# Kernel tuning notes

Measured on AMD Instinct MI355X. Metric: run time of the kernel, lower is better.

The kernel has to match this reference:

```python
import jax, jax.numpy as jnp
import numpy as np

SAMPLE_RATE = 16000
HUM_FREQ = 60
Q_FACTOR = 30.0
BATCH = 128
SAMPLES = 160000


def _notch_sos(freq, Q, fs):
    # scipy.signal.iirnotch closed form (gb = 1/sqrt(2) -> beta = tan(bw/2))
    w0 = 2.0 * np.pi * freq / fs
    beta = np.tan(w0 / (2.0 * Q))
    gain = 1.0 / (1.0 + beta)
    b0 = gain
    b1 = -2.0 * gain * np.cos(w0)
    b2 = gain
    a1 = -2.0 * gain * np.cos(w0)
    a2 = 2.0 * gain - 1.0
    # tf2sos of a 2nd-order TF: single section [b0,b1,b2,a0=1,a1,a2]
    return [b0, b1, b2, 1.0, a1, a2]


def _build_sos():
    rows = []
    for f in (HUM_FREQ, HUM_FREQ * 2, HUM_FREQ * 3):
        if f < SAMPLE_RATE / 2:
            rows.append(_notch_sos(f, Q_FACTOR, SAMPLE_RATE))
    return np.asarray(rows, dtype=np.float32)  # [3, 6]


def setup_inputs() -> dict:
    key = jax.random.key(0)
    audio = jax.random.normal(key, (BATCH, SAMPLES), dtype=jnp.float32)
    sos = jnp.asarray(_build_sos())  # [n_sections, 6], a0 == 1
    return {"audio": audio, "sos": sos}


def _sosfilt(sos, x):
    """Cascaded biquad IIR (direct form II transposed), matching scipy.sosfilt.
    sos: [n_sections, 6] with a0 == 1.  x: [B, T].  Returns [B, T].
    """
    n_sections = sos.shape[0]
    B = x.shape[0]

    def step(z, xt):  # z: [n_sections, 2, B], xt: [B]
        y = xt
        new_z = []
        for s in range(n_sections):
            b0, b1, b2 = sos[s, 0], sos[s, 1], sos[s, 2]
            a1, a2 = sos[s, 4], sos[s, 5]
            out = b0 * y + z[s, 0]
            z0 = b1 * y - a1 * out + z[s, 1]
            z1 = b2 * y - a2 * out
            new_z.append(jnp.stack([z0, z1]))
            y = out
        return jnp.stack(new_z), y

    z_init = jnp.zeros((n_sections, 2, B), dtype=x.dtype)
    _, ys = jax.lax.scan(step, z_init, x.T)  # ys: [T, B]
    return ys.T


def reference(audio, sos):
    squeeze = audio.ndim == 1
    a = audio[None, :] if squeeze else audio
    y = _sosfilt(sos, a)
    return y[0] if squeeze else y
```

## Files before the change

### kernel.cpp

```cpp
#include <hip/hip_runtime.h>

typedef float vfloat4 __attribute__((ext_vector_type(4)));

#define B_ROWS 128
#define T_SAMP 160000
#define NSEC 3
#define LCH 20
#define NF4 5
#define RST 21
#define SUPW 1280
#define NSUP 125
#define NSC (B_ROWS * NSUP)
#define WPB 4

struct Coefs { float b0[NSEC], b1[NSEC], b2[NSEC], a1[NSEC], a2[NSEC]; };

__device__ __forceinline__ void load_coefs(const float* __restrict__ sos, Coefs& c) {
#pragma unroll
  for (int s = 0; s < NSEC; ++s) {
    c.b0[s] = sos[s * 6 + 0];
    c.b1[s] = sos[s * 6 + 1];
    c.b2[s] = sos[s * 6 + 2];
    c.a1[s] = sos[s * 6 + 4];
    c.a2[s] = sos[s * 6 + 5];
  }
}

__device__ __forceinline__ float df2t_step(const Coefs& c, float z[6], float x) {
  float y = x;
#pragma unroll
  for (int s = 0; s < NSEC; ++s) {
    float out = fmaf(c.b0[s], y, z[2 * s]);
    float t0  = fmaf(c.b1[s], y, z[2 * s + 1]);
    z[2 * s]     = fmaf(-c.a1[s], out, t0);
    float t1  = c.b2[s] * y;
    z[2 * s + 1] = fmaf(-c.a2[s], out, t1);
    y = out;
  }
  return y;
}

__device__ __forceinline__ void tri_combine(float f[6], const float* __restrict__ P,
                                            const float t[6]) {
  float nf[6];
#pragma unroll
  for (int e = 0; e < 6; ++e) {
    float acc = f[e];
    const int kmax = ((e >> 1) << 1) + 2;
#pragma unroll
    for (int kk = 0; kk < 6; ++kk)
      if (kk < kmax) acc = fmaf(P[e * 6 + kk], t[kk], acc);
    nf[e] = acc;
  }
#pragma unroll
  for (int e = 0; e < 6; ++e) f[e] = nf[e];
}

__device__ __forceinline__ float dmm6(float a, float b, int i, int j) {
  float s = 0.f;
#pragma unroll
  for (int k = 0; k < 6; ++k)
    s = fmaf(__shfl(a, i * 6 + k), __shfl(b, k * 6 + j), s);
  return s;
}

__global__ __launch_bounds__(64) void setup_kernel(const float* __restrict__ sos,
                                                   float* __restrict__ mats) {
  __shared__ float Ash[36];
  __shared__ float As5[5 * 36];
  const int lane = threadIdx.x;
  Coefs cf; load_coefs(sos, cf);
  if (lane == 0) {
    float A[36];
#pragma unroll
    for (int jc = 0; jc < 6; ++jc) {
      float z[6] = {0.f, 0.f, 0.f, 0.f, 0.f, 0.f};
      z[jc] = 1.f;
      df2t_step(cf, z, 0.f);
#pragma unroll
      for (int ic = 0; ic < 6; ++ic) A[ic * 6 + jc] = z[ic];
    }
#pragma unroll
    for (int q = 0; q < 36; ++q) Ash[q] = A[q];
  }
  __syncthreads();

  const int e = (lane < 36) ? lane : 0;
  const int mi = e / 6, mj = e % 6;
  float a1p = Ash[e];
  float a2p  = dmm6(a1p, a1p, mi, mj);
  float a4p  = dmm6(a2p, a2p, mi, mj);
  float a8p  = dmm6(a4p, a4p, mi, mj);
  float a16p = dmm6(a8p, a8p, mi, mj);
  if (lane < 36) {
    As5[lane] = a1p; As5[36 + lane] = a2p; As5[72 + lane] = a4p;
    As5[108 + lane] = a8p; As5[144 + lane] = a16p;
  }
  float pk = dmm6(a16p, a4p, mi, mj);
  if (lane < 36) mats[lane] = pk;
#pragma unroll
  for (int k = 1; k < 6; ++k) {
    pk = dmm6(pk, pk, mi, mj);
    if (lane < 36) mats[k * 36 + lane] = pk;
  }
  float q = dmm6(pk, pk, mi, mj);
  if (lane < 36) mats[216 + lane] = q;
#pragma unroll
  for (int k = 1; k < 7; ++k) {
    q = dmm6(q, q, mi, mj);
    if (lane < 36) mats[216 + k * 36 + lane] = q;
  }
  if (lane < LCH) {
    float g[6] = {cf.b0[1] * cf.b0[2], 0.f, cf.b0[2], 0.f, 1.f, 0.f};
#pragma unroll
    for (int k = 0; k < 5; ++k) {
      if (lane & (1 << k)) {
        float ng[6];
#pragma unroll
        for (int j = 0; j < 6; ++j) {
          float acc = 0.f;
#pragma unroll
          for (int i = 0; i < 6; ++i) acc = fmaf(g[i], As5[k * 36 + i * 6 + j], acc);
          ng[j] = acc;
        }
#pragma unroll
        for (int j = 0; j < 6; ++j) g[j] = ng[j];
      }
    }
#pragma unroll
    for (int j = 0; j < 6; ++j) mats[468 + lane * 6 + j] = g[j];
  }
}

__global__ __launch_bounds__(256) void pass1_kernel(const float* __restrict__ x,
                                                    const float* __restrict__ sos,
                                                    const float* __restrict__ mats,
                                                    float* __restrict__ Fsup) {
  const int tid = threadIdx.x, w = tid >> 6, lane = tid & 63;
  Coefs cf; load_coefs(sos, cf);
  const int S = blockIdx.x * WPB + w;
  const int r = S / NSUP, s = S - r * NSUP;
  const float4* src = reinterpret_cast<const float4*>(
      x + (size_t)r * T_SAMP + (size_t)s * SUPW + (size_t)lane * LCH);
  float4 v0 = src[0], v1 = src[1], v2 = src[2], v3 = src[3], v4 = src[4];

  float f[6] = {0.f, 0.f, 0.f, 0.f, 0.f, 0.f};
  df2t_step(cf, f, v0.x); df2t_step(cf, f, v0.y); df2t_step(cf, f, v0.z); df2t_step(cf, f, v0.w);
  df2t_step(cf, f, v1.x); df2t_step(cf, f, v1.y); df2t_step(cf, f, v1.z); df2t_step(cf, f, v1.w);
  df2t_step(cf, f, v2.x); df2t_step(cf, f, v2.y); df2t_step(cf, f, v2.z); df2t_step(cf, f, v2.w);
  df2t_step(cf, f, v3.x); df2t_step(cf, f, v3.y); df2t_step(cf, f, v3.z); df2t_step(cf, f, v3.w);
  df2t_step(cf, f, v4.x); df2t_step(cf, f, v4.y); df2t_step(cf, f, v4.z); df2t_step(cf, f, v4.w);

#pragma unroll
  for (int k = 0; k < 6; ++k) {
    float t6[6];
#pragma unroll
    for (int e = 0; e < 6; ++e) t6[e] = __shfl_up(f[e], 1 << k);
    if (lane >= (1 << k)) tri_combine(f, mats + k * 36, t6);
  }
  if (lane == 63) {
    float* fo = Fsup + (size_t)S * 6;
#pragma unroll
    for (int e = 0; e < 6; ++e) fo[e] = f[e];
  }
}

__global__ __launch_bounds__(64) void middle_scan(const float* __restrict__ Fsup,
                                                  const float* __restrict__ mats,
                                                  float* __restrict__ zsup) {
  const float* Qm = mats + 216;
  const int r = blockIdx.x, lane = threadIdx.x;
  const float* frow = Fsup + (size_t)r * NSUP * 6;
  float fc[2][6];
#pragma unroll
  for (int jj = 0; jj < 2; ++jj) {
    int c = 2 * lane + jj;
#pragma unroll
    for (int e = 0; e < 6; ++e) fc[jj][e] = (c < NSUP) ? frow[c * 6 + e] : 0.f;
  }
  float s[6] = {0.f, 0.f, 0.f, 0.f, 0.f, 0.f};
#pragma unroll
  for (int jj = 0; jj < 2; ++jj) {
    float ns[6];
#pragma unroll
    for (int e = 0; e < 6; ++e) {
      float acc = fc[jj][e];
#pragma unroll
      for (int kk = 0; kk < 6; ++kk) acc = fmaf(Qm[e * 6 + kk], s[kk], acc);
      ns[e] = acc;
    }
#pragma unroll
    for (int e = 0; e < 6; ++e) s[e] = ns[e];
  }
#pragma unroll
  for (int k = 0; k < 6; ++k) {
    float t[6];
#pragma unroll
    for (int e = 0; e < 6; ++e) t[e] = __shfl_up(s[e], 1 << k);
    if (lane >= (1 << k)) tri_combine(s, Qm + (k + 1) * 36, t);
  }
  float z[6];
#pragma unroll
  for (int e = 0; e < 6; ++e) {
    float t = __shfl_up(s[e], 1);
    z[e] = (lane == 0) ? 0.f : t;
  }
  float* zrow = zsup + (size_t)r * NSUP * 6;
#pragma unroll
  for (int jj = 0; jj < 2; ++jj) {
    int c = 2 * lane + jj;
    if (c < NSUP) {
#pragma unroll
      for (int e = 0; e < 6; ++e) zrow[c * 6 + e] = z[e];
    }
    float nz[6];
#pragma unroll
    for (int e = 0; e < 6; ++e) {
      float acc = fc[jj][e];
#pragma unroll
      for (int kk = 0; kk < 6; ++kk) acc = fmaf(Qm[e * 6 + kk], z[kk], acc);
      nz[e] = acc;
    }
#pragma unroll
    for (int e = 0; e < 6; ++e) z[e] = nz[e];
  }
}

__global__ __launch_bounds__(256) void pass2_kernel(const float* __restrict__ x,
                                                    const float* __restrict__ sos,
                                                    const float* __restrict__ mats,
                                                    const float* __restrict__ zsup,
                                                    float* __restrict__ y) {
  __shared__ float Tr[WPB][64 * RST];
  const int tid = threadIdx.x, w = tid >> 6, lane = tid & 63;
  Coefs cf; load_coefs(sos, cf);
  const int S = blockIdx.x * WPB + w;
  const int r = S / NSUP, s = S - r * NSUP;
  const size_t base = (size_t)r * T_SAMP + (size_t)s * SUPW;
  const float4* src = reinterpret_cast<const float4*>(x + base + (size_t)lane * LCH);
  float4 v0 = src[0], v1 = src[1], v2 = src[2], v3 = src[3], v4 = src[4];

  float z0[6];
  const float* zp = zsup + (size_t)S * 6;
#pragma unroll
  for (int e = 0; e < 6; ++e) z0[e] = zp[e];

  float f[6] = {0.f, 0.f, 0.f, 0.f, 0.f, 0.f};
  v0.x = df2t_step(cf, f, v0.x); v0.y = df2t_step(cf, f, v0.y);
  v0.z = df2t_step(cf, f, v0.z); v0.w = df2t_step(cf, f, v0.w);
  v1.x = df2t_step(cf, f, v1.x); v1.y = df2t_step(cf, f, v1.y);
  v1.z = df2t_step(cf, f, v1.z); v1.w = df2t_step(cf, f, v1.w);
  v2.x = df2t_step(cf, f, v2.x); v2.y = df2t_step(cf, f, v2.y);
  v2.z = df2t_step(cf, f, v2.z); v2.w = df2t_step(cf, f, v2.w);
  v3.x = df2t_step(cf, f, v3.x); v3.y = df2t_step(cf, f, v3.y);
  v3.z = df2t_step(cf, f, v3.z); v3.w = df2t_step(cf, f, v3.w);
  v4.x = df2t_step(cf, f, v4.x); v4.y = df2t_step(cf, f, v4.y);
  v4.z = df2t_step(cf, f, v4.z); v4.w = df2t_step(cf, f, v4.w);

  if (lane == 0) tri_combine(f, mats, z0);
#pragma unroll
  for (int k = 0; k < 6; ++k) {
    float t6[6];
#pragma unroll
    for (int e = 0; e < 6; ++e) t6[e] = __shfl_up(f[e], 1 << k);
    if (lane >= (1 << k)) tri_combine(f, mats + k * 36, t6);
  }
  float zs[6];
#pragma unroll
  for (int e = 0; e < 6; ++e) {
    float tt = __shfl_up(f[e], 1);
    zs[e] = (lane == 0) ? z0[e] : tt;
  }

  const float* Gm = mats + 468;
  float* myrow = &Tr[w][lane * RST];
  auto corr = [&](int tl, float yz) {
    float a = yz;
#pragma unroll
    for (int e = 0; e < 6; ++e) a = fmaf(Gm[tl * 6 + e], zs[e], a);
    myrow[tl] = a;
  };
  corr(0, v0.x);  corr(1, v0.y);  corr(2, v0.z);  corr(3, v0.w);
  corr(4, v1.x);  corr(5, v1.y);  corr(6, v1.z);  corr(7, v1.w);
  corr(8, v2.x);  corr(9, v2.y);  corr(10, v2.z); corr(11, v2.w);
  corr(12, v3.x); corr(13, v3.y); corr(14, v3.z); corr(15, v3.w);
  corr(16, v4.x); corr(17, v4.y); corr(18, v4.z); corr(19, v4.w);
  __syncthreads();

  float* dst = y + base;
#pragma unroll
  for (int i2 = 0; i2 < NF4; ++i2) {
    int q = i2 * 64 + lane, k = q / NF4, m = q - k * NF4;
    vfloat4 w4;
    w4.x = Tr[w][k * RST + m * 4 + 0];
    w4.y = Tr[w][k * RST + m * 4 + 1];
    w4.z = Tr[w][k * RST + m * 4 + 2];
    w4.w = Tr[w][k * RST + m * 4 + 3];
    __builtin_nontemporal_store(w4, reinterpret_cast<vfloat4*>(dst + 4 * q));
  }
}

extern "C" void kernel_launch(void* const* d_in, const int* in_sizes, int n_in,
                              void* d_out, int out_size, void* d_ws, size_t ws_size,
                              hipStream_t stream) {
  const float* x = (const float*)d_in[0];
  const float* sos = (const float*)d_in[1];
  float* y = (float*)d_out;

  float* Fsup = (float*)d_ws;
  float* zsup = Fsup + (size_t)NSC * 6;
  float* mats = zsup + (size_t)NSC * 6;

  hipLaunchKernelGGL(setup_kernel, dim3(1), dim3(64), 0, stream, sos, mats);
  hipLaunchKernelGGL(pass1_kernel, dim3(NSC / WPB), dim3(256), 0, stream, x, sos, mats, Fsup);
  hipLaunchKernelGGL(middle_scan, dim3(B_ROWS), dim3(64), 0, stream, Fsup, mats, zsup);
  hipLaunchKernelGGL(pass2_kernel, dim3(NSC / WPB), dim3(256), 0, stream, x, sos, mats, zsup, y);
}
```

Baseline: 63.70 us.

## Fuse setup and middle scan into the pass kernels with per-block recompute

Removes the separate setup kernel and the per-row middle scan, leaving two launches. Each block now rebuilds the state-transition matrix powers in shared memory on wave 0, overlapping that with the other waves' chunk filtering. In pass2, each wave finds its incoming state by reducing every earlier superchunk summary in its row with windowed shuffle reductions. This removes two serialized launches and a global round-trip, but repeats the matrix setup in every block and makes pass2 read up to a full row of summaries per wave. The __syncthreads before the transpose store is also dropped, which relies on each wave reading only its own shared-memory slice.

Measured after the change: 103.4 us. 1.62x slower.

```diff
diff --git a/kernel.cpp b/kernel.cpp
--- a/kernel.cpp
+++ b/kernel.cpp
@@ -64,12 +64,21 @@
   return s;
 }
 
-__global__ __launch_bounds__(64) void setup_kernel(const float* __restrict__ sos,
-                                                   float* __restrict__ mats) {
-  __shared__ float Ash[36];
-  __shared__ float As5[5 * 36];
-  const int lane = threadIdx.x;
-  Coefs cf; load_coefs(sos, cf);
+__device__ __forceinline__ void window_reduce(float val[6], const float* __restrict__ Qm,
+                                              int lane) {
+#pragma unroll
+  for (int k = 0; k < 6; ++k) {
+    float t[6];
+#pragma unroll
+    for (int e = 0; e < 6; ++e) t[e] = __shfl_down(val[e], 1 << k);
+    const bool ok = (lane + (1 << k)) < 64;
+#pragma unroll
+    for (int e = 0; e < 6; ++e) t[e] = ok ? t[e] : 0.f;
+    tri_combine(val, Qm + k * 36, t);
+  }
+}
+
+__device__ __forceinline__ float buildA_dist(const Coefs& cf, float* Ash, int lane) {
   if (lane == 0) {
     float A[36];
 #pragma unroll
@@ -83,59 +92,14 @@
 #pragma unroll
     for (int q = 0; q < 36; ++q) Ash[q] = A[q];
   }
-  __syncthreads();
-
-  const int e = (lane < 36) ? lane : 0;
-  const int mi = e / 6, mj = e % 6;
-  float a1p = Ash[e];
-  float a2p  = dmm6(a1p, a1p, mi, mj);
-  float a4p  = dmm6(a2p, a2p, mi, mj);
-  float a8p  = dmm6(a4p, a4p, mi, mj);
-  float a16p = dmm6(a8p, a8p, mi, mj);
-  if (lane < 36) {
-    As5[lane] = a1p; As5[36 + lane] = a2p; As5[72 + lane] = a4p;
-    As5[108 + lane] = a8p; As5[144 + lane] = a16p;
-  }
-  float pk = dmm6(a16p, a4p, mi, mj);
-  if (lane < 36) mats[lane] = pk;
-#pragma unroll
-  for (int k = 1; k < 6; ++k) {
-    pk = dmm6(pk, pk, mi, mj);
-    if (lane < 36) mats[k * 36 + lane] = pk;
-  }
-  float q = dmm6(pk, pk, mi, mj);
-  if (lane < 36) mats[216 + lane] = q;
-#pragma unroll
-  for (int k = 1; k < 7; ++k) {
-    q = dmm6(q, q, mi, mj);
-    if (lane < 36) mats[216 + k * 36 + lane] = q;
-  }
-  if (lane < LCH) {
-    float g[6] = {cf.b0[1] * cf.b0[2], 0.f, cf.b0[2], 0.f, 1.f, 0.f};
-#pragma unroll
-    for (int k = 0; k < 5; ++k) {
-      if (lane & (1 << k)) {
-        float ng[6];
-#pragma unroll
-        for (int j = 0; j < 6; ++j) {
-          float acc = 0.f;
-#pragma unroll
-          for (int i = 0; i < 6; ++i) acc = fmaf(g[i], As5[k * 36 + i * 6 + j], acc);
-          ng[j] = acc;
-        }
-#pragma unroll
-        for (int j = 0; j < 6; ++j) g[j] = ng[j];
-      }
-    }
-#pragma unroll
-    for (int j = 0; j < 6; ++j) mats[468 + lane * 6 + j] = g[j];
-  }
+  return Ash[(lane < 36) ? lane : 0];
 }
 
 __global__ __launch_bounds__(256) void pass1_kernel(const float* __restrict__ x,
                                                     const float* __restrict__ sos,
-                                                    const float* __restrict__ mats,
                                                     float* __restrict__ Fsup) {
+  __shared__ float Ash[36];
+  __shared__ float Pm[6 * 36];
   const int tid = threadIdx.x, w = tid >> 6, lane = tid & 63;
   Coefs cf; load_coefs(sos, cf);
   const int S = blockIdx.x * WPB + w;
@@ -144,19 +108,37 @@
       x + (size_t)r * T_SAMP + (size_t)s * SUPW + (size_t)lane * LCH);
   float4 v0 = src[0], v1 = src[1], v2 = src[2], v3 = src[3], v4 = src[4];
 
+  if (w == 0) {
+    const int e = (lane < 36) ? lane : 0;
+    const int mi = e / 6, mj = e % 6;
+    float a1p = buildA_dist(cf, Ash, lane);
+    float a2p  = dmm6(a1p, a1p, mi, mj);
+    float a4p  = dmm6(a2p, a2p, mi, mj);
+    float a8p  = dmm6(a4p, a4p, mi, mj);
+    float a16p = dmm6(a8p, a8p, mi, mj);
+    float pk = dmm6(a16p, a4p, mi, mj);
+    if (lane < 36) Pm[lane] = pk;
+#pragma unroll
+    for (int k = 1; k < 6; ++k) {
+      pk = dmm6(pk, pk, mi, mj);
+      if (lane < 36) Pm[k * 36 + lane] = pk;
+    }
+  }
+
   float f[6] = {0.f, 0.f, 0.f, 0.f, 0.f, 0.f};
   df2t_step(cf, f, v0.x); df2t_step(cf, f, v0.y); df2t_step(cf, f, v0.z); df2t_step(cf, f, v0.w);
   df2t_step(cf, f, v1.x); df2t_step(cf, f, v1.y); df2t_step(cf, f, v1.z); df2t_step(cf, f, v1.w);
   df2t_step(cf, f, v2.x); df2t_step(cf, f, v2.y); df2t_step(cf, f, v2.z); df2t_step(cf, f, v2.w);
   df2t_step(cf, f, v3.x); df2t_step(cf, f, v3.y); df2t_step(cf, f, v3.z); df2t_step(cf, f, v3.w);
   df2t_step(cf, f, v4.x); df2t_step(cf, f, v4.y); df2t_step(cf, f, v4.z); df2t_step(cf, f, v4.w);
+  __syncthreads();
 
 #pragma unroll
   for (int k = 0; k < 6; ++k) {
     float t6[6];
 #pragma unroll
     for (int e = 0; e < 6; ++e) t6[e] = __shfl_up(f[e], 1 << k);
-    if (lane >= (1 << k)) tri_combine(f, mats + k * 36, t6);
+    if (lane >= (1 << k)) tri_combine(f, Pm + k * 36, t6);
   }
   if (lane == 63) {
     float* fo = Fsup + (size_t)S * 6;
@@ -165,72 +147,15 @@
   }
 }
 
-__global__ __launch_bounds__(64) void middle_scan(const float* __restrict__ Fsup,
-                                                  const float* __restrict__ mats,
-                                                  float* __restrict__ zsup) {
-  const float* Qm = mats + 216;
-  const int r = blockIdx.x, lane = threadIdx.x;
-  const float* frow = Fsup + (size_t)r * NSUP * 6;
-  float fc[2][6];
-#pragma unroll
-  for (int jj = 0; jj < 2; ++jj) {
-    int c = 2 * lane + jj;
-#pragma unroll
-    for (int e = 0; e < 6; ++e) fc[jj][e] = (c < NSUP) ? frow[c * 6 + e] : 0.f;
-  }
-  float s[6] = {0.f, 0.f, 0.f, 0.f, 0.f, 0.f};
-#pragma unroll
-  for (int jj = 0; jj < 2; ++jj) {
-    float ns[6];
-#pragma unroll
-    for (int e = 0; e < 6; ++e) {
-      float acc = fc[jj][e];
-#pragma unroll
-      for (int kk = 0; kk < 6; ++kk) acc = fmaf(Qm[e * 6 + kk], s[kk], acc);
-      ns[e] = acc;
-    }
-#pragma unroll
-    for (int e = 0; e < 6; ++e) s[e] = ns[e];
-  }
-#pragma unroll
-  for (int k = 0; k < 6; ++k) {
-    float t[6];
-#pragma unroll
-    for (int e = 0; e < 6; ++e) t[e] = __shfl_up(s[e], 1 << k);
-    if (lane >= (1 << k)) tri_combine(s, Qm + (k + 1) * 36, t);
-  }
-  float z[6];
-#pragma unroll
-  for (int e = 0; e < 6; ++e) {
-    float t = __shfl_up(s[e], 1);
-    z[e] = (lane == 0) ? 0.f : t;
-  }
-  float* zrow = zsup + (size_t)r * NSUP * 6;
-#pragma unroll
-  for (int jj = 0; jj < 2; ++jj) {
-    int c = 2 * lane + jj;
-    if (c < NSUP) {
-#pragma unroll
-      for (int e = 0; e < 6; ++e) zrow[c * 6 + e] = z[e];
-    }
-    float nz[6];
-#pragma unroll
-    for (int e = 0; e < 6; ++e) {
-      float acc = fc[jj][e];
-#pragma unroll
-      for (int kk = 0; kk < 6; ++kk) acc = fmaf(Qm[e * 6 + kk], z[kk], acc);
-      nz[e] = acc;
-    }
-#pragma unroll
-    for (int e = 0; e < 6; ++e) z[e] = nz[e];
-  }
-}
-
 __global__ __launch_bounds__(256) void pass2_kernel(const float* __restrict__ x,
                                                     const float* __restrict__ sos,
-                                                    const float* __restrict__ mats,
-                                                    const float* __restrict__ zsup,
+                                                    const float* __restrict__ Fsup,
                                                     float* __restrict__ y) {
+  __shared__ float Ash[36];
+  __shared__ float As5[5 * 36];
+  __shared__ float Pm[6 * 36];
+  __shared__ float Qm[7 * 36];
+  __shared__ float Gm[LCH * 6];
   __shared__ float Tr[WPB][64 * RST];
   const int tid = threadIdx.x, w = tid >> 6, lane = tid & 63;
   Coefs cf; load_coefs(sos, cf);
@@ -240,10 +165,53 @@
   const float4* src = reinterpret_cast<const float4*>(x + base + (size_t)lane * LCH);
   float4 v0 = src[0], v1 = src[1], v2 = src[2], v3 = src[3], v4 = src[4];
 
-  float z0[6];
-  const float* zp = zsup + (size_t)S * 6;
-#pragma unroll
-  for (int e = 0; e < 6; ++e) z0[e] = zp[e];
+  if (w == 0) {
+    const int e = (lane < 36) ? lane : 0;
+    const int mi = e / 6, mj = e % 6;
+    float a1p = buildA_dist(cf, Ash, lane);
+    float a2p  = dmm6(a1p, a1p, mi, mj);
+    float a4p  = dmm6(a2p, a2p, mi, mj);
+    float a8p  = dmm6(a4p, a4p, mi, mj);
+    float a16p = dmm6(a8p, a8p, mi, mj);
+    if (lane < 36) {
+      As5[lane] = a1p; As5[36 + lane] = a2p; As5[72 + lane] = a4p;
+      As5[108 + lane] = a8p; As5[144 + lane] = a16p;
+    }
+    float pk = dmm6(a16p, a4p, mi, mj);
+    if (lane < 36) Pm[lane] = pk;
+#pragma unroll
+    for (int k = 1; k < 6; ++k) {
+      pk = dmm6(pk, pk, mi, mj);
+      if (lane < 36) Pm[k * 36 + lane] = pk;
+    }
+    float q = dmm6(pk, pk, mi, mj);
+    if (lane < 36) Qm[lane] = q;
+#pragma unroll
+    for (int k = 1; k < 7; ++k) {
+      q = dmm6(q, q, mi, mj);
+      if (lane < 36) Qm[k * 36 + lane] = q;
+    }
+    if (lane < LCH) {
+      float g[6] = {cf.b0[1] * cf.b0[2], 0.f, cf.b0[2], 0.f, 1.f, 0.f};
+#pragma unroll
+      for (int k = 0; k < 5; ++k) {
+        if (lane & (1 << k)) {
+          float ng[6];
+#pragma unroll
+          for (int j = 0; j < 6; ++j) {
+            float acc = 0.f;
+#pragma unroll
+            for (int i = 0; i < 6; ++i) acc = fmaf(g[i], As5[k * 36 + i * 6 + j], acc);
+            ng[j] = acc;
+          }
+#pragma unroll
+          for (int j = 0; j < 6; ++j) g[j] = ng[j];
+        }
+      }
+#pragma unroll
+      for (int j = 0; j < 6; ++j) Gm[lane * 6 + j] = g[j];
+    }
+  }
 
   float f[6] = {0.f, 0.f, 0.f, 0.f, 0.f, 0.f};
   v0.x = df2t_step(cf, f, v0.x); v0.y = df2t_step(cf, f, v0.y);
@@ -256,14 +224,44 @@
   v3.z = df2t_step(cf, f, v3.z); v3.w = df2t_step(cf, f, v3.w);
   v4.x = df2t_step(cf, f, v4.x); v4.y = df2t_step(cf, f, v4.y);
   v4.z = df2t_step(cf, f, v4.z); v4.w = df2t_step(cf, f, v4.w);
-
-  if (lane == 0) tri_combine(f, mats, z0);
+  __syncthreads();
+
+  float z0[6] = {0.f, 0.f, 0.f, 0.f, 0.f, 0.f};
+  if (s > 0) {
+    const float* frow = Fsup + (size_t)r * NSUP * 6;
+    float acc[6];
+    {
+      const int nv = (s < 64) ? s : 64;
+      const bool act = lane < nv;
+      const int c = s - 1 - lane;
+      float val[6];
+#pragma unroll
+      for (int e = 0; e < 6; ++e) val[e] = act ? frow[c * 6 + e] : 0.f;
+      window_reduce(val, Qm, lane);
+#pragma unroll
+      for (int e = 0; e < 6; ++e) acc[e] = val[e];
+    }
+    if (s > 64) {
+      const int nv = s - 64;
+      const bool act = lane < nv;
+      const int c = s - 65 - lane;
+      float val[6];
+#pragma unroll
+      for (int e = 0; e < 6; ++e) val[e] = act ? frow[c * 6 + e] : 0.f;
+      window_reduce(val, Qm, lane);
+      tri_combine(acc, Qm + 6 * 36, val);
+    }
+#pragma unroll
+    for (int e = 0; e < 6; ++e) z0[e] = __shfl(acc[e], 0);
+  }
+
+  if (lane == 0) tri_combine(f, Pm, z0);
 #pragma unroll
   for (int k = 0; k < 6; ++k) {
     float t6[6];
 #pragma unroll
     for (int e = 0; e < 6; ++e) t6[e] = __shfl_up(f[e], 1 << k);
-    if (lane >= (1 << k)) tri_combine(f, mats + k * 36, t6);
+    if (lane >= (1 << k)) tri_combine(f, Pm + k * 36, t6);
   }
   float zs[6];
 #pragma unroll
@@ -272,7 +270,6 @@
     zs[e] = (lane == 0) ? z0[e] : tt;
   }
 
-  const float* Gm = mats + 468;
   float* myrow = &Tr[w][lane * RST];
   auto corr = [&](int tl, float yz) {
     float a = yz;
@@ -285,7 +282,6 @@
   corr(8, v2.x);  corr(9, v2.y);  corr(10, v2.z); corr(11, v2.w);
   corr(12, v3.x); corr(13, v3.y); corr(14, v3.z); corr(15, v3.w);
   corr(16, v4.x); corr(17, v4.y); corr(18, v4.z); corr(19, v4.w);
-  __syncthreads();
 
   float* dst = y + base;
 #pragma unroll
@@ -308,11 +304,7 @@
   float* y = (float*)d_out;
 
   float* Fsup = (float*)d_ws;
-  float* zsup = Fsup + (size_t)NSC * 6;
-  float* mats = zsup + (size_t)NSC * 6;
-
-  hipLaunchKernelGGL(setup_kernel, dim3(1), dim3(64), 0, stream, sos, mats);
-  hipLaunchKernelGGL(pass1_kernel, dim3(NSC / WPB), dim3(256), 0, stream, x, sos, mats, Fsup);
-  hipLaunchKernelGGL(middle_scan, dim3(B_ROWS), dim3(64), 0, stream, Fsup, mats, zsup);
-  hipLaunchKernelGGL(pass2_kernel, dim3(NSC / WPB), dim3(256), 0, stream, x, sos, mats, zsup, y);
-}
+
+  hipLaunchKernelGGL(pass1_kernel, dim3(NSC / WPB), dim3(256), 0, stream, x, sos, Fsup);
+  hipLaunchKernelGGL(pass2_kernel, dim3(NSC / WPB), dim3(256), 0, stream, x, sos, Fsup, y);
+}
```

## Fold setup kernel into each pass by recomputing transition matrices per block

Applied to the files above, without the earlier changes.

Removes the single-block setup kernel launch and its serial dependency. Each pass instead recomputes the needed transition-matrix powers in shared memory: one wave per block in pass1 and pass2, and the whole block in middle_scan. The recomputation in pass1 and pass2 overlaps with the other waves' local filtering before a block barrier. The cost is redundant shuffle-based matrix products in every block, plus an extra barrier placed before the scan.

After: 69.64 us. 9.3% more time.

```diff
diff --git a/kernel.cpp b/kernel.cpp
--- a/kernel.cpp
+++ b/kernel.cpp
@@ -64,12 +64,7 @@
   return s;
 }
 
-__global__ __launch_bounds__(64) void setup_kernel(const float* __restrict__ sos,
-                                                   float* __restrict__ mats) {
-  __shared__ float Ash[36];
-  __shared__ float As5[5 * 36];
-  const int lane = threadIdx.x;
-  Coefs cf; load_coefs(sos, cf);
+__device__ __forceinline__ float buildA_dist(const Coefs& cf, float* Ash, int lane) {
   if (lane == 0) {
     float A[36];
 #pragma unroll
@@ -83,59 +78,14 @@
 #pragma unroll
     for (int q = 0; q < 36; ++q) Ash[q] = A[q];
   }
-  __syncthreads();
-
-  const int e = (lane < 36) ? lane : 0;
-  const int mi = e / 6, mj = e % 6;
-  float a1p = Ash[e];
-  float a2p  = dmm6(a1p, a1p, mi, mj);
-  float a4p  = dmm6(a2p, a2p, mi, mj);
-  float a8p  = dmm6(a4p, a4p, mi, mj);
-  float a16p = dmm6(a8p, a8p, mi, mj);
-  if (lane < 36) {
-    As5[lane] = a1p; As5[36 + lane] = a2p; As5[72 + lane] = a4p;
-    As5[108 + lane] = a8p; As5[144 + lane] = a16p;
-  }
-  float pk = dmm6(a16p, a4p, mi, mj);
-  if (lane < 36) mats[lane] = pk;
-#pragma unroll
-  for (int k = 1; k < 6; ++k) {
-    pk = dmm6(pk, pk, mi, mj);
-    if (lane < 36) mats[k * 36 + lane] = pk;
-  }
-  float q = dmm6(pk, pk, mi, mj);
-  if (lane < 36) mats[216 + lane] = q;
-#pragma unroll
-  for (int k = 1; k < 7; ++k) {
-    q = dmm6(q, q, mi, mj);
-    if (lane < 36) mats[216 + k * 36 + lane] = q;
-  }
-  if (lane < LCH) {
-    float g[6] = {cf.b0[1] * cf.b0[2], 0.f, cf.b0[2], 0.f, 1.f, 0.f};
-#pragma unroll
-    for (int k = 0; k < 5; ++k) {
-      if (lane & (1 << k)) {
-        float ng[6];
-#pragma unroll
-        for (int j = 0; j < 6; ++j) {
-          float acc = 0.f;
-#pragma unroll
-          for (int i = 0; i < 6; ++i) acc = fmaf(g[i], As5[k * 36 + i * 6 + j], acc);
-          ng[j] = acc;
-        }
-#pragma unroll
-        for (int j = 0; j < 6; ++j) g[j] = ng[j];
-      }
-    }
-#pragma unroll
-    for (int j = 0; j < 6; ++j) mats[468 + lane * 6 + j] = g[j];
-  }
+  return Ash[(lane < 36) ? lane : 0];
 }
 
 __global__ __launch_bounds__(256) void pass1_kernel(const float* __restrict__ x,
                                                     const float* __restrict__ sos,
-                                                    const float* __restrict__ mats,
                                                     float* __restrict__ Fsup) {
+  __shared__ float Ash[36];
+  __shared__ float Pm[6 * 36];
   const int tid = threadIdx.x, w = tid >> 6, lane = tid & 63;
   Coefs cf; load_coefs(sos, cf);
   const int S = blockIdx.x * WPB + w;
@@ -144,19 +94,37 @@
       x + (size_t)r * T_SAMP + (size_t)s * SUPW + (size_t)lane * LCH);
   float4 v0 = src[0], v1 = src[1], v2 = src[2], v3 = src[3], v4 = src[4];
 
+  if (w == 0) {
+    const int e = (lane < 36) ? lane : 0;
+    const int mi = e / 6, mj = e % 6;
+    float a1p = buildA_dist(cf, Ash, lane);
+    float a2p  = dmm6(a1p, a1p, mi, mj);
+    float a4p  = dmm6(a2p, a2p, mi, mj);
+    float a8p  = dmm6(a4p, a4p, mi, mj);
+    float a16p = dmm6(a8p, a8p, mi, mj);
+    float pk = dmm6(a16p, a4p, mi, mj);
+    if (lane < 36) Pm[lane] = pk;
+#pragma unroll
+    for (int k = 1; k < 6; ++k) {
+      pk = dmm6(pk, pk, mi, mj);
+      if (lane < 36) Pm[k * 36 + lane] = pk;
+    }
+  }
+
   float f[6] = {0.f, 0.f, 0.f, 0.f, 0.f, 0.f};
   df2t_step(cf, f, v0.x); df2t_step(cf, f, v0.y); df2t_step(cf, f, v0.z); df2t_step(cf, f, v0.w);
   df2t_step(cf, f, v1.x); df2t_step(cf, f, v1.y); df2t_step(cf, f, v1.z); df2t_step(cf, f, v1.w);
   df2t_step(cf, f, v2.x); df2t_step(cf, f, v2.y); df2t_step(cf, f, v2.z); df2t_step(cf, f, v2.w);
   df2t_step(cf, f, v3.x); df2t_step(cf, f, v3.y); df2t_step(cf, f, v3.z); df2t_step(cf, f, v3.w);
   df2t_step(cf, f, v4.x); df2t_step(cf, f, v4.y); df2t_step(cf, f, v4.z); df2t_step(cf, f, v4.w);
+  __syncthreads();
 
 #pragma unroll
   for (int k = 0; k < 6; ++k) {
     float t6[6];
 #pragma unroll
     for (int e = 0; e < 6; ++e) t6[e] = __shfl_up(f[e], 1 << k);
-    if (lane >= (1 << k)) tri_combine(f, mats + k * 36, t6);
+    if (lane >= (1 << k)) tri_combine(f, Pm + k * 36, t6);
   }
   if (lane == 63) {
     float* fo = Fsup + (size_t)S * 6;
@@ -166,10 +134,32 @@
 }
 
 __global__ __launch_bounds__(64) void middle_scan(const float* __restrict__ Fsup,
-                                                  const float* __restrict__ mats,
+                                                  const float* __restrict__ sos,
                                                   float* __restrict__ zsup) {
-  const float* Qm = mats + 216;
+  __shared__ float Ash[36];
+  __shared__ float Qm[7 * 36];
   const int r = blockIdx.x, lane = threadIdx.x;
+  Coefs cf; load_coefs(sos, cf);
+  {
+    const int e = (lane < 36) ? lane : 0;
+    const int mi = e / 6, mj = e % 6;
+    float a1p = buildA_dist(cf, Ash, lane);
+    float a2p  = dmm6(a1p, a1p, mi, mj);
+    float a4p  = dmm6(a2p, a2p, mi, mj);
+    float a8p  = dmm6(a4p, a4p, mi, mj);
+    float a16p = dmm6(a8p, a8p, mi, mj);
+    float m = dmm6(a16p, a4p, mi, mj);
+#pragma unroll
+    for (int k = 0; k < 6; ++k) m = dmm6(m, m, mi, mj);
+    if (lane < 36) Qm[lane] = m;
+#pragma unroll
+    for (int k = 1; k < 7; ++k) {
+      m = dmm6(m, m, mi, mj);
+      if (lane < 36) Qm[k * 36 + lane] = m;
+    }
+  }
+  __syncthreads();
+
   const float* frow = Fsup + (size_t)r * NSUP * 6;
   float fc[2][6];
 #pragma unroll
@@ -228,9 +218,12 @@
 
 __global__ __launch_bounds__(256) void pass2_kernel(const float* __restrict__ x,
                                                     const float* __restrict__ sos,
-                                                    const float* __restrict__ mats,
                                                     const float* __restrict__ zsup,
                                                     float* __restrict__ y) {
+  __shared__ float Ash[36];
+  __shared__ float As5[5 * 36];
+  __shared__ float Pm[6 * 36];
+  __shared__ float Gm[LCH * 6];
   __shared__ float Tr[WPB][64 * RST];
   const int tid = threadIdx.x, w = tid >> 6, lane = tid & 63;
   Coefs cf; load_coefs(sos, cf);
@@ -244,6 +237,47 @@
   const float* zp = zsup + (size_t)S * 6;
 #pragma unroll
   for (int e = 0; e < 6; ++e) z0[e] = zp[e];
+
+  if (w == 0) {
+    const int e = (lane < 36) ? lane : 0;
+    const int mi = e / 6, mj = e % 6;
+    float a1p = buildA_dist(cf, Ash, lane);
+    float a2p  = dmm6(a1p, a1p, mi, mj);
+    float a4p  = dmm6(a2p, a2p, mi, mj);
+    float a8p  = dmm6(a4p, a4p, mi, mj);
+    float a16p = dmm6(a8p, a8p, mi, mj);
+    if (lane < 36) {
+      As5[lane] = a1p; As5[36 + lane] = a2p; As5[72 + lane] = a4p;
+      As5[108 + lane] = a8p; As5[144 + lane] = a16p;
+    }
+    float pk = dmm6(a16p, a4p, mi, mj);
+    if (lane < 36) Pm[lane] = pk;
+#pragma unroll
+    for (int k = 1; k < 6; ++k) {
+      pk = dmm6(pk, pk, mi, mj);
+      if (lane < 36) Pm[k * 36 + lane] = pk;
+    }
+    if (lane < LCH) {
+      float g[6] = {cf.b0[1] * cf.b0[2], 0.f, cf.b0[2], 0.f, 1.f, 0.f};
+#pragma unroll
+      for (int k = 0; k < 5; ++k) {
+        if (lane & (1 << k)) {
+          float ng[6];
+#pragma unroll
+          for (int j = 0; j < 6; ++j) {
+            float acc = 0.f;
+#pragma unroll
+            for (int i = 0; i < 6; ++i) acc = fmaf(g[i], As5[k * 36 + i * 6 + j], acc);
+            ng[j] = acc;
+          }
+#pragma unroll
+          for (int j = 0; j < 6; ++j) g[j] = ng[j];
+        }
+      }
+#pragma unroll
+      for (int j = 0; j < 6; ++j) Gm[lane * 6 + j] = g[j];
+    }
+  }
 
   float f[6] = {0.f, 0.f, 0.f, 0.f, 0.f, 0.f};
   v0.x = df2t_step(cf, f, v0.x); v0.y = df2t_step(cf, f, v0.y);
@@ -256,14 +290,15 @@
   v3.z = df2t_step(cf, f, v3.z); v3.w = df2t_step(cf, f, v3.w);
   v4.x = df2t_step(cf, f, v4.x); v4.y = df2t_step(cf, f, v4.y);
   v4.z = df2t_step(cf, f, v4.z); v4.w = df2t_step(cf, f, v4.w);
-
-  if (lane == 0) tri_combine(f, mats, z0);
+  __syncthreads();
+
+  if (lane == 0) tri_combine(f, Pm, z0);
 #pragma unroll
   for (int k = 0; k < 6; ++k) {
     float t6[6];
 #pragma unroll
     for (int e = 0; e < 6; ++e) t6[e] = __shfl_up(f[e], 1 << k);
-    if (lane >= (1 << k)) tri_combine(f, mats + k * 36, t6);
+    if (lane >= (1 << k)) tri_combine(f, Pm + k * 36, t6);
   }
   float zs[6];
 #pragma unroll
@@ -272,7 +307,6 @@
     zs[e] = (lane == 0) ? z0[e] : tt;
   }
 
-  const float* Gm = mats + 468;
   float* myrow = &Tr[w][lane * RST];
   auto corr = [&](int tl, float yz) {
     float a = yz;
@@ -285,7 +319,6 @@
   corr(8, v2.x);  corr(9, v2.y);  corr(10, v2.z); corr(11, v2.w);
   corr(12, v3.x); corr(13, v3.y); corr(14, v3.z); corr(15, v3.w);
   corr(16, v4.x); corr(17, v4.y); corr(18, v4.z); corr(19, v4.w);
-  __syncthreads();
 
   float* dst = y + base;
 #pragma unroll
@@ -309,10 +342,8 @@
 
   float* Fsup = (float*)d_ws;
   float* zsup = Fsup + (size_t)NSC * 6;
-  float* mats = zsup + (size_t)NSC * 6;
-
-  hipLaunchKernelGGL(setup_kernel, dim3(1), dim3(64), 0, stream, sos, mats);
-  hipLaunchKernelGGL(pass1_kernel, dim3(NSC / WPB), dim3(256), 0, stream, x, sos, mats, Fsup);
-  hipLaunchKernelGGL(middle_scan, dim3(B_ROWS), dim3(64), 0, stream, Fsup, mats, zsup);
-  hipLaunchKernelGGL(pass2_kernel, dim3(NSC / WPB), dim3(256), 0, stream, x, sos, mats, zsup, y);
-}
+
+  hipLaunchKernelGGL(pass1_kernel, dim3(NSC / WPB), dim3(256), 0, stream, x, sos, Fsup);
+  hipLaunchKernelGGL(middle_scan, dim3(B_ROWS), dim3(64), 0, stream, Fsup, sos, zsup);
+  hipLaunchKernelGGL(pass2_kernel, dim3(NSC / WPB), dim3(256), 0, stream, x, sos, zsup, y);
+}
```
